# Kernel optimization log

Hardware: AMD Instinct MI355X
Metric: run time of the kernel (lower is better)

Reference implementation:

```python
import jax, jax.numpy as jnp
import numpy as np

BN_EPS = 1e-5


def _conv(x, w):
    # x: [N, Cin, H, W], w: [Cout, Cin, kh, kw], stride 1, padding 1 (same for 3x3)
    return jax.lax.conv_general_dilated(
        x, w, window_strides=(1, 1), padding=[(1, 1), (1, 1)],
        dimension_numbers=('NCHW', 'OIHW', 'NCHW'))


def setup_inputs() -> dict:
    key = jax.random.key(0)
    ks = jax.random.split(key, 4)
    T, N, Cin, Cout, H, W = 16, 4, 64, 64, 64, 64
    x = jax.random.normal(ks[0], (T, N, Cin, H, W), dtype=jnp.float32)
    # conv_x2h: Conv2d(Cin, 4*Cout, k=3, s=1, p=1, bias=True) + BatchNorm2d(4*Cout)
    Wx = jax.random.normal(ks[1], (4 * Cout, Cin, 3, 3), dtype=jnp.float32) * 0.05
    bx = jax.random.normal(ks[2], (4 * Cout,), dtype=jnp.float32) * 0.05
    gamma = jnp.ones((4 * Cout,), dtype=jnp.float32)
    beta = jnp.zeros((4 * Cout,), dtype=jnp.float32)
    # conv_h2h: Conv2d(Cout, 4*Cout, k=3, p=1, bias=False)
    Wh = jax.random.normal(ks[3], (4 * Cout, Cout, 3, 3), dtype=jnp.float32) * 0.05
    return {"x": x, "Wx": Wx, "bx": bx, "gamma": gamma, "beta": beta, "Wh": Wh}


def reference(x, Wx, bx, gamma, beta, Wh):
    T, N, Cin, H, W = x.shape
    hidden = Wh.shape[1]

    # ---- SequenceWise(Conv2d + BatchNorm(train) + Identity) ----
    xf = x.reshape(T * N, Cin, H, W)
    y = _conv(xf, Wx) + bx[None, :, None, None]
    mean = jnp.mean(y, axis=(0, 2, 3))
    var = jnp.var(y, axis=(0, 2, 3))  # biased, as torch BN uses for normalization
    y = (y - mean[None, :, None, None]) * jax.lax.rsqrt(var[None, :, None, None] + BN_EPS)
    y = y * gamma[None, :, None, None] + beta[None, :, None, None]
    y = y.reshape(T, N, 4 * hidden, H, W)

    # ---- ConvLSTMCell recurrence over time ----
    # zeros init is exactly equivalent to prev_h/prev_c = None:
    # conv_h2h(0) = 0 (no bias) and f*0 + i*g = i*g.
    h0 = jnp.zeros((N, hidden, H, W), dtype=x.dtype)
    c0 = jnp.zeros((N, hidden, H, W), dtype=x.dtype)

    def step(carry, xt):
        h, c = carry
        tmp = _conv(h, Wh) + xt
        cc_i, cc_f, cc_o, cc_g = jnp.split(tmp, 4, axis=1)
        i = jax.nn.sigmoid(cc_i)
        f = jax.nn.sigmoid(cc_f)
        o = jax.nn.sigmoid(cc_o)
        g = jnp.tanh(cc_g)
        c = f * c + i * g
        h = o * jnp.tanh(c)
        return (h, c), h

    _, hs = jax.lax.scan(step, (h0, c0), y)
    return hs  # [T, N, hidden, H, W]
```

## Files before the change

### kernel.cpp

```cpp
#include <hip/hip_runtime.h>
#include <hip/hip_bf16.h>

typedef float        f32x4  __attribute__((ext_vector_type(4)));
typedef unsigned int u32x4  __attribute__((ext_vector_type(4)));
typedef __bf16       bf16x8 __attribute__((ext_vector_type(8)));

__device__ __forceinline__ unsigned short f2bf(float f) {
    unsigned u = __builtin_bit_cast(unsigned, f);
    u += 0x7fffu + ((u >> 16) & 1u);
    return (unsigned short)(u >> 16);
}
__device__ __forceinline__ float bf2f(unsigned short u) {
    union { unsigned ui; float f; } c; c.ui = ((unsigned)u) << 16; return c.f;
}
__device__ __forceinline__ void gload_lds16(const void* g, void* l) {
    __builtin_amdgcn_global_load_lds(
        (const __attribute__((address_space(1))) unsigned int*)g,
        (__attribute__((address_space(3))) unsigned int*)l, 16, 0, 0);
}

__global__ __launch_bounds__(256) void k_xT(const float* __restrict__ x,
                                            unsigned short* __restrict__ xT) {
    __shared__ unsigned int tl[256 * 32];
    const int img = blockIdx.x >> 4;
    const int p0  = (blockIdx.x & 15) * 256;
    const int tid = threadIdx.x;
    const float* xi = x + (size_t)img * 64 * 4096 + p0 + tid;
#pragma unroll
    for (int cp = 0; cp < 32; ++cp) {
        float a = xi[(size_t)(2 * cp) * 4096];
        float b = xi[(size_t)(2 * cp + 1) * 4096];
        unsigned v = (unsigned)f2bf(a) | ((unsigned)f2bf(b) << 16);
        tl[tid * 32 + (cp ^ (tid & 31))] = v;
    }
    __syncthreads();
    unsigned short* dst = xT + ((size_t)img * 4096 + p0) * 64;
#pragma unroll
    for (int k = 0; k < 8; ++k) {
        int c = tid + k * 256;
        int pix = c >> 3, slot = c & 7;
        unsigned w[4];
#pragma unroll
        for (int i = 0; i < 4; ++i)
            w[i] = tl[pix * 32 + ((slot * 4 + i) ^ (pix & 31))];
        *(u32x4*)(dst + (size_t)pix * 64 + slot * 8) = *(u32x4*)w;
    }
}

__global__ __launch_bounds__(256) void k_pack2(const float* __restrict__ Wx,
                                               const float* __restrict__ Wh,
                                               unsigned short* __restrict__ Axp,
                                               unsigned short* __restrict__ Ahp) {
    int b = blockIdx.x;
    const float* W = (b < 576) ? Wx : Wh;
    unsigned short* Ap = (b < 576) ? Axp : Ahp;
    int idx = (b % 576) * 256 + threadIdx.x;
    if (idx >= 256 * 576) return;
    int row = idx / 576, k = idx % 576;
    int kb = k / 288, r2 = k % 288;
    int tap = r2 / 32, w32 = r2 % 32;
    int s = w32 >> 3, e = w32 & 7;
    int ci = kb * 32 + ((s ^ (row & 3)) << 3) + e;
    int co = (row & 3) * 64 + (row >> 2);
    Ap[idx] = f2bf(W[((size_t)co * 64 + ci) * 9 + tap]);
}

__global__ __launch_bounds__(256) void k_conv0(
    const unsigned short* __restrict__ src,
    const unsigned short* __restrict__ Ap,
    unsigned short* __restrict__ ybf,
    float2* __restrict__ prt)
{
    constexpr int TH = 16, N_ = 4, HR = 18;

    __shared__ __align__(16) unsigned short halo[HR * 18 * 64];
    __shared__ __align__(16) unsigned short As[2][2048];

    const int bid  = blockIdx.x;
    const int xcd  = bid & 7;
    const int sidx = bid >> 3;
    const int grp  = sidx & 3;
    const int pairG = (sidx >> 2) * 8 + xcd;
    const int tile = pairG & 15;
    const int img  = pairG >> 4;
    const int py0 = (tile >> 2) * TH, px0 = (tile & 3) * 16;
    const int tid = threadIdx.x;
    const int wv = tid >> 6, lane = tid & 63;
    const int cl = lane & 15, q = lane >> 4;
    const int rowbase = grp * 64;

    f32x4 acc[4][N_];
#pragma unroll
    for (int m = 0; m < 4; ++m)
#pragma unroll
        for (int n = 0; n < N_; ++n)
            acc[m][n] = (f32x4){0.f, 0.f, 0.f, 0.f};

    {
        const char* agp = (const char*)Ap +
            (size_t)(rowbase + (tid >> 2)) * 1152 + (tid & 3) * 16;
        gload_lds16(agp, (char*)&As[0][0] + tid * 16);

        const unsigned short* sb = src + (size_t)img * 4096 * 64;
        char* hB = (char*)halo;
        for (int tau = tid; tau < HR * 144; tau += 256) {
            int s = tau & 7, hcc = (tau >> 3) % 18, hrr = tau / 144;
            int gy = py0 + hrr - 1, gx = px0 + hcc - 1;
            u32x4 v = {0u, 0u, 0u, 0u};
            if ((unsigned)gy < 64u && (unsigned)gx < 64u)
                v = *(const u32x4*)(sb + ((gy * 64 + gx) * 64 + s * 8));
            *(u32x4*)(hB + (hrr * 18 + hcc) * 128 + ((s * 16) ^ ((hcc & 7) << 4))) = v;
        }
        __syncthreads();

        int aoff[4];
#pragma unroll
        for (int m = 0; m < 4; ++m)
            aoff[m] = (m * 16 + cl) * 64 + ((q * 16) ^ ((cl & 3) << 4));

        const char* AsRd = (const char*)&As[0][0];
#pragma unroll
        for (int ks = 0; ks < 18; ++ks) {
            const int buf = ks & 1;
            if (ks < 17)
                gload_lds16(agp + (ks + 1) * 64, (char*)&As[buf ^ 1][0] + tid * 16);

            const int kb = ks / 9, tap = ks % 9;
            const int ky = tap / 3, kx = tap - ky * 3;

            u32x4 af[4];
#pragma unroll
            for (int m = 0; m < 4; ++m)
                af[m] = *(const u32x4*)(AsRd + buf * 4096 + aoff[m]);

            int hcv  = cl + kx;
            int cbase = hcv * 128 + ((kb * 64 + q * 16) ^ ((hcv & 7) << 4));
            __builtin_amdgcn_s_setprio(1);
#pragma unroll
            for (int n = 0; n < N_; ++n) {
                int hr = wv * N_ + n + ky;
                u32x4 bv = *(const u32x4*)(hB + hr * 2304 + cbase);
                bf16x8 bfr = __builtin_bit_cast(bf16x8, bv);
#pragma unroll
                for (int m = 0; m < 4; ++m)
                    acc[m][n] = __builtin_amdgcn_mfma_f32_16x16x32_bf16(
                        __builtin_bit_cast(bf16x8, af[m]), bfr, acc[m][n], 0, 0, 0);
            }
            __builtin_amdgcn_s_setprio(0);
            __syncthreads();
        }
    }

#pragma unroll
    for (int m = 0; m < 4; ++m) {
#pragma unroll
        for (int n = 0; n < N_; ++n) {
            int pix = (py0 + wv * N_ + n) * 64 + px0 + cl;
            uint2 w;
            w.x = (unsigned)f2bf(acc[m][n][0]) | ((unsigned)f2bf(acc[m][n][1]) << 16);
            w.y = (unsigned)f2bf(acc[m][n][2]) | ((unsigned)f2bf(acc[m][n][3]) << 16);
            *(uint2*)(ybf + ((size_t)img * 4096 + pix) * 256 + rowbase + m * 16 + q * 4) = w;
        }
    }
    float* bnred = (float*)halo;
#pragma unroll
    for (int m = 0; m < 4; ++m) {
#pragma unroll
        for (int j = 0; j < 4; ++j) {
            float s = 0.f, qq = 0.f;
#pragma unroll
            for (int n = 0; n < N_; ++n) {
                float v = acc[m][n][j];
                s += v; qq += v * v;
            }
#pragma unroll
            for (int mask = 1; mask <= 8; mask <<= 1) {
                s  += __shfl_xor(s,  mask, 64);
                qq += __shfl_xor(qq, mask, 64);
            }
            if (cl == 0) {
                int ci_ = (wv * 4 + q) * 16 + m * 4 + j;
                bnred[ci_ * 2]     = s;
                bnred[ci_ * 2 + 1] = qq;
            }
        }
    }
    __syncthreads();
    if (tid < 64) {
        int m_ = tid >> 4, qj = tid & 15;
        float s = 0.f, qq = 0.f;
#pragma unroll
        for (int w = 0; w < 4; ++w) {
            int idx = ((w * 4 + (qj >> 2)) * 16 + m_ * 4 + (qj & 3)) * 2;
            s += bnred[idx]; qq += bnred[idx + 1];
        }
        prt[(size_t)(rowbase + tid) * 1024 + img * 16 + tile] = make_float2(s, qq);
    }
}

__global__ __launch_bounds__(256) void k_bn_fin(
    const float2* __restrict__ prt, const float* __restrict__ bx,
    const float* __restrict__ gamma, const float* __restrict__ beta,
    float* __restrict__ ss) {
    int c = blockIdx.x;
    const float2* p = prt + (size_t)c * 1024;
    float s = 0.f, sq = 0.f;
    for (int i = threadIdx.x; i < 1024; i += 256) {
        float2 v = p[i]; s += v.x; sq += v.y;
    }
    __shared__ float rs[256], rq[256];
    int tid = threadIdx.x;
    rs[tid] = s; rq[tid] = sq;
    __syncthreads();
    for (int off = 128; off > 0; off >>= 1) {
        if (tid < off) { rs[tid] += rs[tid + off]; rq[tid] += rq[tid + off]; }
        __syncthreads();
    }
    if (tid == 0) {
        int co = (c & 3) * 64 + (c >> 2);
        float mean = rs[0] * (1.f / 262144.f);
        float var  = rq[0] * (1.f / 262144.f) - mean * mean;
        float sc   = gamma[co] * rsqrtf(var + 1e-5f);
        ss[c]       = sc;
        ss[256 + c] = beta[co] - mean * sc;
        (void)bx;
    }
}

__global__ __launch_bounds__(256) void k_step(
    const unsigned short* __restrict__ hin,
    const unsigned short* __restrict__ Ap,
    const unsigned short* __restrict__ ybf,
    const float* __restrict__ ss,
    float* __restrict__ cst,
    unsigned short* __restrict__ hout,
    float* __restrict__ out,
    int t, int first)
{
    constexpr int TH = 8, N_ = 2, HR = 10;

    __shared__ __align__(16) unsigned short halo[HR * 18 * 64];
    __shared__ __align__(16) unsigned short As[2][2048];

    const int bid  = blockIdx.x;
    const int xcd  = bid & 7;
    const int sidx = bid >> 3;
    const int grp  = sidx & 3;
    const int pairG = (sidx >> 2) * 8 + xcd;
    const int tile = pairG & 31;
    const int img  = pairG >> 5;
    const int py0 = (tile >> 2) * TH, px0 = (tile & 3) * 16;
    const int tid = threadIdx.x;
    const int wv = tid >> 6, lane = tid & 63;
    const int cl = lane & 15, q = lane >> 4;
    const int rowbase = grp * 64;

    uint2 ypre[4][N_];
    float cpre[4][N_];
#pragma unroll
    for (int m = 0; m < 4; ++m) {
        int hc = grp * 16 + m * 4 + q;
#pragma unroll
        for (int n = 0; n < N_; ++n) {
            int pix = (py0 + wv * N_ + n) * 64 + px0 + cl;
            ypre[m][n] = *(const uint2*)(ybf +
                ((size_t)(t * 4 + img) * 4096 + pix) * 256 + hc * 4);
            cpre[m][n] = first ? 0.f : cst[((size_t)img * 64 + hc) * 4096 + pix];
        }
    }

    f32x4 acc[4][N_];
#pragma unroll
    for (int m = 0; m < 4; ++m)
#pragma unroll
        for (int n = 0; n < N_; ++n)
            acc[m][n] = (f32x4){0.f, 0.f, 0.f, 0.f};

    if (!first) {
        const char* agp = (const char*)Ap +
            (size_t)(rowbase + (tid >> 2)) * 1152 + (tid & 3) * 16;
        gload_lds16(agp, (char*)&As[0][0] + tid * 16);

        const unsigned short* sb = hin + (size_t)img * 4096 * 64;
        char* hB = (char*)halo;
        for (int tau = tid; tau < HR * 144; tau += 256) {
            int s = tau & 7, hcc = (tau >> 3) % 18, hrr = tau / 144;
            int gy = py0 + hrr - 1, gx = px0 + hcc - 1;
            u32x4 v = {0u, 0u, 0u, 0u};
            if ((unsigned)gy < 64u && (unsigned)gx < 64u)
                v = *(const u32x4*)(sb + ((gy * 64 + gx) * 64 + s * 8));
            *(u32x4*)(hB + (hrr * 18 + hcc) * 128 + ((s * 16) ^ ((hcc & 7) << 4))) = v;
        }
        __syncthreads();

        int aoff[4];
#pragma unroll
        for (int m = 0; m < 4; ++m)
            aoff[m] = (m * 16 + cl) * 64 + ((q * 16) ^ ((cl & 3) << 4));

        const char* AsRd = (const char*)&As[0][0];
#pragma unroll
        for (int ks = 0; ks < 18; ++ks) {
            const int buf = ks & 1;
            if (ks < 17)
                gload_lds16(agp + (ks + 1) * 64, (char*)&As[buf ^ 1][0] + tid * 16);

            const int kb = ks / 9, tap = ks % 9;
            const int ky = tap / 3, kx = tap - ky * 3;

            u32x4 af[4];
#pragma unroll
            for (int m = 0; m < 4; ++m)
                af[m] = *(const u32x4*)(AsRd + buf * 4096 + aoff[m]);

            int hcv  = cl + kx;
            int cbase = hcv * 128 + ((kb * 64 + q * 16) ^ ((hcv & 7) << 4));
            __builtin_amdgcn_s_setprio(1);
#pragma unroll
            for (int n = 0; n < N_; ++n) {
                int hr = wv * N_ + n + ky;
                u32x4 bv = *(const u32x4*)(hB + hr * 2304 + cbase);
                bf16x8 bfr = __builtin_bit_cast(bf16x8, bv);
#pragma unroll
                for (int m = 0; m < 4; ++m)
                    acc[m][n] = __builtin_amdgcn_mfma_f32_16x16x32_bf16(
                        __builtin_bit_cast(bf16x8, af[m]), bfr, acc[m][n], 0, 0, 0);
            }
            __builtin_amdgcn_s_setprio(0);
            __syncthreads();
        }
    }

    unsigned short* hbounce = halo;
    const f32x4* sc4 = (const f32x4*)ss;
    const f32x4* sh4 = (const f32x4*)(ss + 256);
#pragma unroll
    for (int m = 0; m < 4; ++m) {
        int hc = grp * 16 + m * 4 + q;
        f32x4 sc = sc4[hc], sh = sh4[hc];
#pragma unroll
        for (int n = 0; n < N_; ++n) {
            int pix = (py0 + wv * N_ + n) * 64 + px0 + cl;
            uint2 yv = ypre[m][n];
            float tmp[4];
            tmp[0] = acc[m][n][0] + sc[0] * bf2f((unsigned short)(yv.x & 0xffffu)) + sh[0];
            tmp[1] = acc[m][n][1] + sc[1] * bf2f((unsigned short)(yv.x >> 16))     + sh[1];
            tmp[2] = acc[m][n][2] + sc[2] * bf2f((unsigned short)(yv.y & 0xffffu)) + sh[2];
            tmp[3] = acc[m][n][3] + sc[3] * bf2f((unsigned short)(yv.y >> 16))     + sh[3];
            float iv = 1.f / (1.f + __expf(-tmp[0]));
            float fv = 1.f / (1.f + __expf(-tmp[1]));
            float ov = 1.f / (1.f + __expf(-tmp[2]));
            float e2 = __expf(2.f * tmp[3]);
            float gv = 1.f - 2.f / (e2 + 1.f);
            size_t cidx = ((size_t)img * 64 + hc) * 4096 + pix;
            float cnew = fv * cpre[m][n] + iv * gv;
            cst[cidx] = cnew;
            float e2c = __expf(2.f * cnew);
            float hv  = ov * (1.f - 2.f / (e2c + 1.f));
            out[((size_t)(t * 4 + img) * 64 + hc) * 4096 + pix] = hv;
            hbounce[((wv * N_ + n) * 16 + cl) * 16 + m * 4 + q] = f2bf(hv);
        }
    }
    __syncthreads();
    if (tid < TH * 16) {
        int pixg = (py0 + (tid >> 4)) * 64 + px0 + (tid & 15);
        u32x4* dst = (u32x4*)(hout + ((size_t)img * 4096 + pixg) * 64 + grp * 16);
        u32x4* s0  = (u32x4*)(hbounce + tid * 16);
        dst[0] = s0[0];
        dst[1] = s0[1];
    }
}

extern "C" void kernel_launch(void* const* d_in, const int* in_sizes, int n_in,
                              void* d_out, int out_size, void* d_ws, size_t ws_size,
                              hipStream_t stream) {
    const float* x     = (const float*)d_in[0];
    const float* Wx    = (const float*)d_in[1];
    const float* bx    = (const float*)d_in[2];
    const float* gamma = (const float*)d_in[3];
    const float* beta  = (const float*)d_in[4];
    const float* Wh    = (const float*)d_in[5];
    float* out = (float*)d_out;

    char* ws = (char*)d_ws;
    unsigned short* y   = (unsigned short*)ws;
    unsigned short* Axp = (unsigned short*)(ws + 134217728);
    unsigned short* Ahp = (unsigned short*)(ws + 134512640);
    float*          ss  = (float*)(ws + 134807552);
    float*          cs  = (float*)(ws + 134809600);
    float2*         prt = (float2*)(ws + 139003904);
    unsigned short* hA  = (unsigned short*)(ws + 139003904);
    unsigned short* hB  = (unsigned short*)(ws + 141101056);

    unsigned short* xT = (unsigned short*)d_out;

    k_xT   <<<1024, 256, 0, stream>>>(x, xT);
    k_pack2<<<1152, 256, 0, stream>>>(Wx, Wh, Axp, Ahp);

    k_conv0<<<4096, 256, 0, stream>>>(xT, Axp, y, prt);
    k_bn_fin<<<256, 256, 0, stream>>>(prt, bx, gamma, beta, ss);

    unsigned short* hbuf[2] = {hA, hB};
    for (int t = 0; t < 16; ++t) {
        k_step<<<512, 256, 0, stream>>>(hbuf[t & 1], Ahp, y, ss, cs,
                                        hbuf[(t + 1) & 1], out, t, t == 0 ? 1 : 0);
    }
}
```

Measured before the change: 388.3 us.

## Widen conv0 blocks to 128 output channels to share halo loads

```diff
diff --git a/kernel.cpp b/kernel.cpp
--- a/kernel.cpp
+++ b/kernel.cpp
@@ -65,35 +65,37 @@
     Ap[idx] = f2bf(W[((size_t)co * 64 + ci) * 9 + tap]);
 }
 
-__global__ __launch_bounds__(256) void k_conv0(
+__global__ __launch_bounds__(512) void k_conv0(
     const unsigned short* __restrict__ src,
     const unsigned short* __restrict__ Ap,
     unsigned short* __restrict__ ybf,
     float2* __restrict__ prt)
 {
-    constexpr int TH = 16, N_ = 4, HR = 18;
+    constexpr int HR = 18;
 
     __shared__ __align__(16) unsigned short halo[HR * 18 * 64];
-    __shared__ __align__(16) unsigned short As[2][2048];
+    __shared__ __align__(16) unsigned short As[2][128 * 32];
 
     const int bid  = blockIdx.x;
     const int xcd  = bid & 7;
     const int sidx = bid >> 3;
-    const int grp  = sidx & 3;
-    const int pairG = (sidx >> 2) * 8 + xcd;
+    const int grp2 = sidx & 1;
+    const int pairG = (sidx >> 1) * 8 + xcd;
     const int tile = pairG & 15;
     const int img  = pairG >> 4;
-    const int py0 = (tile >> 2) * TH, px0 = (tile & 3) * 16;
+    const int py0 = (tile >> 2) * 16, px0 = (tile & 3) * 16;
     const int tid = threadIdx.x;
-    const int wv = tid >> 6, lane = tid & 63;
+    const int wv = tid >> 6;
+    const int rgrp = wv >> 2, wq = wv & 3;
+    const int lane = tid & 63;
     const int cl = lane & 15, q = lane >> 4;
-    const int rowbase = grp * 64;
-
-    f32x4 acc[4][N_];
+    const int rowbase = grp2 * 128;
+
+    f32x4 acc[4][4];
 #pragma unroll
     for (int m = 0; m < 4; ++m)
 #pragma unroll
-        for (int n = 0; n < N_; ++n)
+        for (int n = 0; n < 4; ++n)
             acc[m][n] = (f32x4){0.f, 0.f, 0.f, 0.f};
 
     {
@@ -103,7 +105,7 @@
 
         const unsigned short* sb = src + (size_t)img * 4096 * 64;
         char* hB = (char*)halo;
-        for (int tau = tid; tau < HR * 144; tau += 256) {
+        for (int tau = tid; tau < HR * 144; tau += 512) {
             int s = tau & 7, hcc = (tau >> 3) % 18, hrr = tau / 144;
             int gy = py0 + hrr - 1, gx = px0 + hcc - 1;
             u32x4 v = {0u, 0u, 0u, 0u};
@@ -116,7 +118,7 @@
         int aoff[4];
 #pragma unroll
         for (int m = 0; m < 4; ++m)
-            aoff[m] = (m * 16 + cl) * 64 + ((q * 16) ^ ((cl & 3) << 4));
+            aoff[m] = (rgrp * 64 + m * 16 + cl) * 64 + ((q * 16) ^ ((cl & 3) << 4));
 
         const char* AsRd = (const char*)&As[0][0];
 #pragma unroll
@@ -131,14 +133,13 @@
             u32x4 af[4];
 #pragma unroll
             for (int m = 0; m < 4; ++m)
-                af[m] = *(const u32x4*)(AsRd + buf * 4096 + aoff[m]);
+                af[m] = *(const u32x4*)(AsRd + buf * 8192 + aoff[m]);
 
             int hcv  = cl + kx;
             int cbase = hcv * 128 + ((kb * 64 + q * 16) ^ ((hcv & 7) << 4));
-            __builtin_amdgcn_s_setprio(1);
-#pragma unroll
-            for (int n = 0; n < N_; ++n) {
-                int hr = wv * N_ + n + ky;
+#pragma unroll
+            for (int n = 0; n < 4; ++n) {
+                int hr = wq * 4 + n + ky;
                 u32x4 bv = *(const u32x4*)(hB + hr * 2304 + cbase);
                 bf16x8 bfr = __builtin_bit_cast(bf16x8, bv);
 #pragma unroll
@@ -146,20 +147,20 @@
                     acc[m][n] = __builtin_amdgcn_mfma_f32_16x16x32_bf16(
                         __builtin_bit_cast(bf16x8, af[m]), bfr, acc[m][n], 0, 0, 0);
             }
-            __builtin_amdgcn_s_setprio(0);
             __syncthreads();
         }
     }
 
 #pragma unroll
     for (int m = 0; m < 4; ++m) {
-#pragma unroll
-        for (int n = 0; n < N_; ++n) {
-            int pix = (py0 + wv * N_ + n) * 64 + px0 + cl;
+        int co = rowbase + rgrp * 64 + m * 16 + q * 4;
+#pragma unroll
+        for (int n = 0; n < 4; ++n) {
+            int pix = (py0 + wq * 4 + n) * 64 + px0 + cl;
             uint2 w;
             w.x = (unsigned)f2bf(acc[m][n][0]) | ((unsigned)f2bf(acc[m][n][1]) << 16);
             w.y = (unsigned)f2bf(acc[m][n][2]) | ((unsigned)f2bf(acc[m][n][3]) << 16);
-            *(uint2*)(ybf + ((size_t)img * 4096 + pix) * 256 + rowbase + m * 16 + q * 4) = w;
+            *(uint2*)(ybf + ((size_t)img * 4096 + pix) * 256 + co) = w;
         }
     }
     float* bnred = (float*)halo;
@@ -169,7 +170,7 @@
         for (int j = 0; j < 4; ++j) {
             float s = 0.f, qq = 0.f;
 #pragma unroll
-            for (int n = 0; n < N_; ++n) {
+            for (int n = 0; n < 4; ++n) {
                 float v = acc[m][n][j];
                 s += v; qq += v * v;
             }
@@ -179,19 +180,19 @@
                 qq += __shfl_xor(qq, mask, 64);
             }
             if (cl == 0) {
-                int ci_ = (wv * 4 + q) * 16 + m * 4 + j;
+                int ci_ = ((rgrp * 4 + wq) * 4 + q) * 16 + m * 4 + j;
                 bnred[ci_ * 2]     = s;
                 bnred[ci_ * 2 + 1] = qq;
             }
         }
     }
     __syncthreads();
-    if (tid < 64) {
-        int m_ = tid >> 4, qj = tid & 15;
+    if (tid < 128) {
+        int rg = tid >> 6, m_ = (tid >> 4) & 3, qj = tid & 15;
         float s = 0.f, qq = 0.f;
 #pragma unroll
         for (int w = 0; w < 4; ++w) {
-            int idx = ((w * 4 + (qj >> 2)) * 16 + m_ * 4 + (qj & 3)) * 2;
+            int idx = (((rg * 4 + w) * 4 + (qj >> 2)) * 16 + m_ * 4 + (qj & 3)) * 2;
             s += bnred[idx]; qq += bnred[idx + 1];
         }
         prt[(size_t)(rowbase + tid) * 1024 + img * 16 + tile] = make_float2(s, qq);
@@ -315,7 +316,6 @@
 
             int hcv  = cl + kx;
             int cbase = hcv * 128 + ((kb * 64 + q * 16) ^ ((hcv & 7) << 4));
-            __builtin_amdgcn_s_setprio(1);
 #pragma unroll
             for (int n = 0; n < N_; ++n) {
                 int hr = wv * N_ + n + ky;
@@ -326,7 +326,6 @@
                     acc[m][n] = __builtin_amdgcn_mfma_f32_16x16x32_bf16(
                         __builtin_bit_cast(bf16x8, af[m]), bfr, acc[m][n], 0, 0, 0);
             }
-            __builtin_amdgcn_s_setprio(0);
             __syncthreads();
         }
     }
@@ -397,7 +396,7 @@
     k_xT   <<<1024, 256, 0, stream>>>(x, xT);
     k_pack2<<<1152, 256, 0, stream>>>(Wx, Wh, Axp, Ahp);
 
-    k_conv0<<<4096, 256, 0, stream>>>(xT, Axp, y, prt);
+    k_conv0<<<2048, 512, 0, stream>>>(xT, Axp, y, prt);
     k_bn_fin<<<256, 256, 0, stream>>>(prt, bx, gamma, beta, ss);
 
     unsigned short* hbuf[2] = {hA, hB};
```

Result: faster. 378.8 us (-2.5%).
